# Kernel optimization log

Measured on AMD Instinct MI355X. Metric: run time of the kernel, lower is better.

The kernel has to match this reference:

```python
import jax, jax.numpy as jnp
import numpy as np

B, S, H = 2, 2048, 1024
NQ, NKV, HD, RANK = 16, 4, 64, 8
THETA = 10000.0
LORA_SCALE = 16 / RANK  # alpha / rank = 2.0
ATTN_SCALE = 1.0 / np.sqrt(HD)


def setup_inputs() -> dict:
    key = jax.random.key(0)
    ks = jax.random.split(key, 14)
    n = lambda k, shape, s: jax.random.normal(k, shape, jnp.float32) * s
    return {
        "x": n(ks[0], (B, S, H), 1.0),
        # nn.Linear weights: [out_features, in_features], y = x @ W.T (scaled small for stability)
        "Wq": n(ks[1], (NQ * HD, H), 0.02),
        "Wk": n(ks[2], (NKV * HD, H), 0.02),
        "Wv": n(ks[3], (NKV * HD, H), 0.02),
        "Wo": n(ks[4], (H, NQ * HD), 0.02),
        "qA": n(ks[5], (RANK, H), 0.05), "qB": n(ks[6], (NQ * HD, RANK), 0.05),
        "kA": n(ks[7], (RANK, H), 0.05), "kB": n(ks[8], (NKV * HD, RANK), 0.05),
        "vA": n(ks[9], (RANK, H), 0.05), "vB": n(ks[10], (NKV * HD, RANK), 0.05),
        "oA": n(ks[11], (RANK, NQ * HD), 0.05), "oB": n(ks[12], (H, RANK), 0.05),
    }


def _lora_proj(x, W, A, Bm):
    # x @ W.T + ((x @ A.T) @ B.T) * lora_scaling
    return x @ W.T + ((x @ A.T) @ Bm.T) * LORA_SCALE


def _rope(x, cos_h, sin_h):
    # x: [b, h, s, d]; even/odd interleaved split, concatenated output (matches torch ref)
    x1, x2 = x[..., ::2], x[..., 1::2]
    return jnp.concatenate([x1 * cos_h - x2 * sin_h, x1 * sin_h + x2 * cos_h], axis=-1)


def _forward(x, Wq, Wk, Wv, Wo, qA, qB, kA, kB, vA, vB, oA, oB):
    b, s, _ = x.shape
    q = _lora_proj(x, Wq, qA, qB).reshape(b, s, NQ, HD).transpose(0, 2, 1, 3)
    k = _lora_proj(x, Wk, kA, kB).reshape(b, s, NKV, HD).transpose(0, 2, 1, 3)
    v = _lora_proj(x, Wv, vA, vB).reshape(b, s, NKV, HD).transpose(0, 2, 1, 3)

    inv_freq = 1.0 / (THETA ** (jnp.arange(0, HD, 2, dtype=jnp.float32) / HD))  # [HD/2]
    freqs = jnp.arange(s, dtype=jnp.float32)[:, None] * inv_freq[None, :]  # [s, HD/2]
    cos_h = jnp.cos(freqs)[None, None]  # [1,1,s,HD/2]
    sin_h = jnp.sin(freqs)[None, None]
    q = _rope(q, cos_h, sin_h)
    k = _rope(k, cos_h, sin_h)

    rep = NQ // NKV  # GQA: repeat_interleave along head axis
    k = jnp.repeat(k, rep, axis=1)
    v = jnp.repeat(v, rep, axis=1)

    attn = jax.nn.softmax(jnp.einsum('bhqd,bhkd->bhqk', q, k) * ATTN_SCALE, axis=-1)
    out = jnp.einsum('bhqk,bhkd->bhqd', attn, v)
    out = out.transpose(0, 2, 1, 3).reshape(b, s, NQ * HD)
    return _lora_proj(out, Wo, oA, oB)


def reference(x, Wq, Wk, Wv, Wo, qA, qB, kA, kB, vA, vB, oA, oB):
    return _forward(x, Wq, Wk, Wv, Wo, qA, qB, kA, kB, vA, vB, oA, oB)
```

## Files before the change

kernel.cpp:

```cpp
#include <hip/hip_runtime.h>

typedef _Float16 f16;
typedef __attribute__((ext_vector_type(8))) _Float16 f16x8;
typedef __attribute__((ext_vector_type(4))) float f32x4;

#define DI __device__ __forceinline__
#define MFMA16(a, b, c) __builtin_amdgcn_mfma_f32_16x16x32_f16(a, b, c, 0, 0, 0)

constexpr int BB = 2, SS = 2048, HH = 1024;
constexpr int NQ = 16, NKV = 4, HD = 64;
constexpr int NTOK = BB * SS;
constexpr int NQKV = NQ*HD + 2*NKV*HD;

DI f32x4 zero4() { f32x4 z = {0.f, 0.f, 0.f, 0.f}; return z; }

DI float fexp2(float x) {
#if __has_builtin(__builtin_amdgcn_exp2f)
  return __builtin_amdgcn_exp2f(x);
#else
  return exp2f(x);
#endif
}

DI unsigned pk2(float a, float b) {
#if __has_builtin(__builtin_amdgcn_cvt_pkrtz)
  typedef __fp16 fp16v2 __attribute__((ext_vector_type(2)));
  union { fp16v2 h; unsigned u; } c;
  c.h = __builtin_amdgcn_cvt_pkrtz(a, b);
  return c.u;
#else
  union { f16 h[2]; unsigned u; } c;
  c.h[0] = (f16)a; c.h[1] = (f16)b; return c.u;
#endif
}

DI void glds16(const void* g, void* l) {
  __builtin_amdgcn_global_load_lds((const __attribute__((address_space(1))) void*)g,
                                   (__attribute__((address_space(3))) void*)l, 16, 0, 0);
}

DI int shuf32(int i) {
  return (i & ~31) | (((i >> 2) & 3) << 3) | (i & 3) | (((i >> 4) & 1) << 2);
}

DI void store4h(f16* dst, float4 v) {
  union { f16 h[4]; uint2 u; } o;
  o.h[0] = (f16)v.x; o.h[1] = (f16)v.y; o.h[2] = (f16)v.z; o.h[3] = (f16)v.w;
  *reinterpret_cast<uint2*>(dst) = o.u;
}

__global__ __launch_bounds__(256) void prep_kernel(
    const float* __restrict__ x,
    const float* __restrict__ Wq, const float* __restrict__ Wk,
    const float* __restrict__ Wv, const float* __restrict__ Wo,
    const float* __restrict__ qA, const float* __restrict__ qB,
    const float* __restrict__ kA, const float* __restrict__ kB,
    const float* __restrict__ vA, const float* __restrict__ vB,
    const float* __restrict__ oA, const float* __restrict__ oB,
    f16* __restrict__ xh, f16* __restrict__ Wqkv, f16* __restrict__ Woe,
    float* __restrict__ ctab, float* __restrict__ stab) {
  int u = blockIdx.x * 256 + threadIdx.x;
  if (u < 393216) {
    int e = u << 2;
    int n = e >> 10, hc = e & 1023;
    const float *Am, *Bm; const float* Wsrc; int nn;
    if (n < 1024)      { nn = n;        Wsrc = Wq + e;              Am = qA; Bm = qB; }
    else if (n < 1280) { nn = n - 1024; Wsrc = Wk + nn*1024 + hc;   Am = kA; Bm = kB; }
    else               { nn = n - 1280; Wsrc = Wv + nn*1024 + hc;   Am = vA; Bm = vB; }
    float4 wv = *reinterpret_cast<const float4*>(Wsrc);
    float4 s = {0.f, 0.f, 0.f, 0.f};
#pragma unroll
    for (int r = 0; r < 8; ++r) {
      float bw = 2.0f * Bm[nn*8 + r];
      float4 av = *reinterpret_cast<const float4*>(Am + r*1024 + hc);
      s.x += bw*av.x; s.y += bw*av.y; s.z += bw*av.z; s.w += bw*av.w;
    }
    wv.x += s.x; wv.y += s.y; wv.z += s.z; wv.w += s.w;
    store4h(Wqkv + shuf32(e), wv);
  } else if ((u -= 393216) < 262144) {
    int e = u << 2;
    int n = e >> 10, hc = e & 1023;
    float4 wv = *reinterpret_cast<const float4*>(Wo + e);
    float4 s = {0.f, 0.f, 0.f, 0.f};
#pragma unroll
    for (int r = 0; r < 8; ++r) {
      float bw = 2.0f * oB[n*8 + r];
      float4 av = *reinterpret_cast<const float4*>(oA + r*1024 + hc);
      s.x += bw*av.x; s.y += bw*av.y; s.z += bw*av.z; s.w += bw*av.w;
    }
    wv.x += s.x; wv.y += s.y; wv.z += s.z; wv.w += s.w;
    store4h(Woe + shuf32(e), wv);
  } else if ((u -= 262144) < 1048576) {
    int e = u << 2;
    float4 v = *reinterpret_cast<const float4*>(x + e);
    store4h(xh + shuf32(e), v);
  } else if ((u -= 1048576) < SS * 32) {
    int s = u >> 5, d = u & 31;
    float inv = expf(-(float)d * 0.28782313662425583f);
    float ang = (float)s * inv;
    ctab[u] = cosf(ang);
    stab[u] = sinf(ang);
  }
}

template<typename OUT_T, int BN>
__global__ __launch_bounds__(256, 3) void gemm_bt(const f16* __restrict__ A, const f16* __restrict__ Bw,
                                                  OUT_T* __restrict__ C, int M, int N, int K) {
  constexpr int BUFB = 16384 + BN * 128;
  __shared__ char lds[2 * BUFB];
  const int nt = N / BN;
  const int nwg = (M >> 7) * nt;
  int bid = blockIdx.x;
  const int cpx = nwg >> 3;
  bid = (bid & 7) * cpx + (bid >> 3);
  const int m0 = (bid / nt) << 7;
  const int n0 = (bid % nt) * BN;
  const int tid = threadIdx.x;
  const int lane = tid & 63;
  const int w = tid >> 6;
  const int wr = (BN == 128) ? (w >> 1) : w;
  const int wc = (BN == 128) ? (w & 1) : 0;
  constexpr int MI = (BN == 128) ? 4 : 2;
  const int l15 = lane & 15, g = (lane >> 4) & 3;
  const char* Ab = (const char*)A;
  const char* Bb = (const char*)Bw;
  const size_t Kb = (size_t)K * 2;
  const int srow = tid >> 3;
  const int scol = (tid & 7) << 4;

  auto stage = [&](int kt, int bs) {
    char* ab = lds + bs * BUFB;
    char* bbuf = ab + 16384;
    const size_t kbyte = (size_t)kt << 7;
#pragma unroll
    for (int s = 0; s < 4; ++s) {
      int row = (s << 5) + srow;
      glds16(Ab + (size_t)(m0 + row) * Kb + kbyte + (scol ^ ((row & 7) << 4)),
             ab + (s << 12) + (w << 10));
    }
#pragma unroll
    for (int s = 0; s < BN / 32; ++s) {
      int row = (s << 5) + srow;
      glds16(Bb + (size_t)(n0 + row) * Kb + kbyte + (scol ^ ((row & 7) << 4)),
             bbuf + (s << 12) + (w << 10));
    }
  };

  f32x4 acc[MI][4];
#pragma unroll
  for (int i = 0; i < MI; ++i)
#pragma unroll
    for (int j = 0; j < 4; ++j) acc[i][j] = zero4();

  const int nkt = K >> 6;
  stage(0, 0);
  for (int t = 0; t < nkt; ++t) {
    __syncthreads();
    if (t + 1 < nkt) stage(t + 1, (t + 1) & 1);
    const char* ab = lds + (t & 1) * BUFB;
    const char* bbuf = ab + 16384;
    f16x8 af[MI][2], bf[4][2];
#pragma unroll
    for (int mi = 0; mi < MI; ++mi) {
      int ra = wr * (MI << 4) + (mi << 4) + l15;
      int base = ra << 7, sw = (ra & 7) << 4;
#pragma unroll
      for (int kk = 0; kk < 2; ++kk)
        af[mi][kk] = *reinterpret_cast<const f16x8*>(ab + base + ((((kk << 6) + (g << 4))) ^ sw));
    }
#pragma unroll
    for (int nj = 0; nj < 4; ++nj) {
      int rb = (wc << 6) + (nj << 4) + l15;
      int base = rb << 7, sw = (rb & 7) << 4;
#pragma unroll
      for (int kk = 0; kk < 2; ++kk)
        bf[nj][kk] = *reinterpret_cast<const f16x8*>(bbuf + base + ((((kk << 6) + (g << 4))) ^ sw));
    }
#pragma unroll
    for (int mi = 0; mi < MI; ++mi)
#pragma unroll
      for (int nj = 0; nj < 4; ++nj) {
        acc[mi][nj] = MFMA16(af[mi][0], bf[nj][0], acc[mi][nj]);
        acc[mi][nj] = MFMA16(af[mi][1], bf[nj][1], acc[mi][nj]);
      }
  }
#pragma unroll
  for (int mi = 0; mi < MI; ++mi)
#pragma unroll
    for (int nj = 0; nj < 4; ++nj) {
      int mmb = m0 + wr * (MI << 4) + (mi << 4) + (g << 2);
      int nn  = n0 + (wc << 6) + (nj << 4) + l15;
      f32x4 a = acc[mi][nj];
#pragma unroll
      for (int r = 0; r < 4; ++r) C[(size_t)(mmb + r) * N + nn] = (OUT_T)a[r];
    }
}

__global__ __launch_bounds__(256) void ropev_kernel(const f16* __restrict__ qkv,
    const float* __restrict__ ctab, const float* __restrict__ stab,
    f16* __restrict__ Qr, f16* __restrict__ Kr, f16* __restrict__ Vt) {
  __shared__ f16 Ls[64 * 72];
  if (blockIdx.x < 2560) {
    int u = blockIdx.x * 256 + threadIdx.x;
    int j = u & 7;
    int t = u >> 3;
    int hh = t % 20;
    int tok = t / 20;
    int s = tok & (SS - 1), b = tok >> 11;
    float4 cs = *reinterpret_cast<const float4*>(ctab + (s << 5) + (j << 2));
    float4 sn = *reinterpret_cast<const float4*>(stab + (s << 5) + (j << 2));
    const f16* src = qkv + (size_t)tok * NQKV + (hh < 16 ? hh*64 : 1024 + (hh - 16)*64) + (j << 3);
    union { uint4 q; f16 h[8]; } v;
    v.q = *reinterpret_cast<const uint4*>(src);
    const float sc = hh < 16 ? 0.18033688011112042f : 1.0f;
    f16* out = (hh < 16) ? (Qr + ((size_t)(b*NQ + hh)*SS + s) * HD)
                         : (Kr + ((size_t)(b*NKV + hh - 16)*SS + s) * HD);
    float cc[4] = {cs.x, cs.y, cs.z, cs.w};
    float ss[4] = {sn.x, sn.y, sn.z, sn.w};
    union { f16 h[4]; uint2 u2; } o1, o2;
#pragma unroll
    for (int e = 0; e < 4; ++e) {
      float x1 = (float)v.h[2*e], x2 = (float)v.h[2*e + 1];
      o1.h[e] = (f16)(sc * (x1*cc[e] - x2*ss[e]));
      o2.h[e] = (f16)(sc * (x1*ss[e] + x2*cc[e]));
    }
    int p1b = ((j & 3) << 3) + ((j >> 2) << 2);
    *reinterpret_cast<uint2*>(out + p1b) = o1.u2;
    *reinterpret_cast<uint2*>(out + p1b + 32) = o2.u2;
  } else {
    const int tid = threadIdx.x;
    const int blk = blockIdx.x - 2560;
    const int st = blk & 31, hkv = (blk >> 5) & 3, b = blk >> 7;
    const int s0 = st << 6;
    {
      int s = tid >> 2, d0 = (tid & 3) << 4;
      const f16* src = qkv + ((size_t)(b*SS + s0 + s)) * NQKV + 1280 + hkv*64 + d0;
      uint4 v0 = *reinterpret_cast<const uint4*>(src);
      uint4 v1 = *reinterpret_cast<const uint4*>(src + 8);
      *reinterpret_cast<uint4*>(Ls + s * 72 + d0) = v0;
      *reinterpret_cast<uint4*>(Ls + s * 72 + d0 + 8) = v1;
    }
    __syncthreads();
    int d = tid >> 2;
    f16* dst = Vt + ((size_t)(b*NKV + hkv)*64 + d) * SS + s0;
#pragma unroll
    for (int cc = 0; cc < 2; ++cc) {
      int cch = ((tid & 3) << 1) + cc;
      int m = cch >> 2, g = cch & 3;
      union { f16 h[8]; uint4 u; } o;
#pragma unroll
      for (int j = 0; j < 8; ++j) {
        int sl = (m << 5) + (g << 2) + (j & 3) + ((j >> 2) << 4);
        o.h[j] = Ls[sl * 72 + d];
      }
      *reinterpret_cast<uint4*>(dst + (cch << 3)) = o.u;
    }
  }
}

__global__ __launch_bounds__(512, 4) void attn_kernel(
    const f16* __restrict__ Qr, const f16* __restrict__ Kr,
    const f16* __restrict__ Vt, f16* __restrict__ AO) {
  __shared__ char lds[3 * 16384];
  const int tid = threadIdx.x, lane = tid & 63, w = tid >> 6;
  const int l15 = lane & 15, g = (lane >> 4) & 3;
  const int bh = blockIdx.x;
  const int b = bh >> 4, h = bh & 15, hkv = h >> 2;
  const int q0 = blockIdx.y << 8;
  const char* Kbase = (const char*)(Kr + (size_t)(b*NKV + hkv) * SS * HD);
  const char* Vbase = (const char*)(Vt + (size_t)(b*NKV + hkv) * HD * SS);

  f16x8 qf[2][2];
  {
    const f16* qr0 = Qr + ((size_t)(b*NQ + h)*SS + q0 + (w << 5) + l15) * HD + (g << 3);
    qf[0][0] = *reinterpret_cast<const f16x8*>(qr0);
    qf[0][1] = *reinterpret_cast<const f16x8*>(qr0 + 32);
    qf[1][0] = *reinterpret_cast<const f16x8*>(qr0 + 16*HD);
    qf[1][1] = *reinterpret_cast<const f16x8*>(qr0 + 16*HD + 32);
  }
  f16x8 ones;
#pragma unroll
  for (int i = 0; i < 8; ++i) ones[i] = (f16)1.0f;
  const f32x4 minit = {-4.f, -4.f, -4.f, -4.f};

  f32x4 acc[4][2];
#pragma unroll
  for (int i = 0; i < 4; ++i) { acc[i][0] = zero4(); acc[i][1] = zero4(); }
  f32x4 es0 = zero4(), es1 = zero4();

  f16x8 vreg[4][2];
  union { unsigned u[8]; f16x8 v[2]; } p0, p1;

  const int srow = tid >> 3;
  const int scolb = (tid & 7) << 4;
  auto stage = [&](int kv0, int buf) {
    char* kb = lds + buf * 16384;
    char* vb = kb + 8192;
    glds16(Kbase + (size_t)(kv0 + srow) * 128 + (scolb ^ ((srow & 7) << 4)),
           kb + (w << 10));
    glds16(Vbase + (size_t)srow * 4096 + (kv0 << 1) + (scolb ^ ((srow & 7) << 4)),
           vb + (w << 10));
  };

  stage(0, 0);
  stage(64, 1);
  int cur = 0;

  for (int t = 0; t < 32; ++t) {
    if (t < 31) asm volatile("s_waitcnt vmcnt(2)" ::: "memory");
    else        asm volatile("s_waitcnt vmcnt(0)" ::: "memory");
    __builtin_amdgcn_s_barrier();
    __builtin_amdgcn_sched_barrier(0);
    int nb = cur + 2; if (nb >= 3) nb -= 3;
    if (t + 2 < 32) stage((t + 2) << 6, nb);

    const char* kb = lds + cur * 16384;
    const char* vb = kb + 8192;

    __builtin_amdgcn_s_setprio(1);
    if (t > 0) {
#pragma unroll
      for (int sh = 0; sh < 2; ++sh) {
#pragma unroll
        for (int db = 0; db < 4; ++db) {
          acc[db][0] = MFMA16(vreg[db][sh], p0.v[sh], acc[db][0]);
          acc[db][1] = MFMA16(vreg[db][sh], p1.v[sh], acc[db][1]);
        }
        es0 = MFMA16(ones, p0.v[sh], es0);
        es1 = MFMA16(ones, p1.v[sh], es1);
      }
    }
#pragma unroll
    for (int mb = 0; mb < 4; ++mb) {
      int rowK = (mb << 4) + l15;
      int Bk = (rowK << 7) + ((g << 4) ^ ((rowK & 7) << 4));
      f16x8 kf0 = *reinterpret_cast<const f16x8*>(kb + Bk);
      f16x8 kf1 = *reinterpret_cast<const f16x8*>(kb + (Bk ^ 64));
      f32x4 z0 = minit, z1 = minit;
      z0 = MFMA16(kf0, qf[0][0], z0); z0 = MFMA16(kf1, qf[0][1], z0);
      z1 = MFMA16(kf0, qf[1][0], z1); z1 = MFMA16(kf1, qf[1][1], z1);
      p0.u[(mb << 1)]     = pk2(fexp2(z0[0]), fexp2(z0[1]));
      p0.u[(mb << 1) + 1] = pk2(fexp2(z0[2]), fexp2(z0[3]));
      p1.u[(mb << 1)]     = pk2(fexp2(z1[0]), fexp2(z1[1]));
      p1.u[(mb << 1) + 1] = pk2(fexp2(z1[2]), fexp2(z1[3]));
    }
    __builtin_amdgcn_s_setprio(0);
#pragma unroll
    for (int db = 0; db < 4; ++db) {
      int rowV = (db << 4) + l15;
      int Bv = (rowV << 7) + ((g << 4) ^ ((rowV & 7) << 4));
      vreg[db][0] = *reinterpret_cast<const f16x8*>(vb + Bv);
      vreg[db][1] = *reinterpret_cast<const f16x8*>(vb + (Bv ^ 64));
    }
    cur += 1; if (cur == 3) cur = 0;
  }
#pragma unroll
  for (int sh = 0; sh < 2; ++sh) {
#pragma unroll
    for (int db = 0; db < 4; ++db) {
      acc[db][0] = MFMA16(vreg[db][sh], p0.v[sh], acc[db][0]);
      acc[db][1] = MFMA16(vreg[db][sh], p1.v[sh], acc[db][1]);
    }
    es0 = MFMA16(ones, p0.v[sh], es0);
    es1 = MFMA16(ones, p1.v[sh], es1);
  }

  float i0 = 1.0f / es0[0], i1 = 1.0f / es1[0];
  int sg0 = q0 + (w << 5) + l15;
  size_t ob0 = ((size_t)b * SS + sg0) * 1024 + h * 64;
  size_t ob1 = ob0 + (size_t)16 * 1024;
#pragma unroll
  for (int db = 0; db < 4; ++db) {
    union { f16 hv[4]; uint2 u; } o0, o1;
#pragma unroll
    for (int r = 0; r < 4; ++r) {
      o0.hv[r] = (f16)(acc[db][0][r] * i0);
      o1.hv[r] = (f16)(acc[db][1][r] * i1);
    }
    int pos = ((db >> 1) << 5) + (g << 3) + ((db & 1) << 2);
    *reinterpret_cast<uint2*>(AO + ob0 + pos) = o0.u;
    *reinterpret_cast<uint2*>(AO + ob1 + pos) = o1.u;
  }
}

extern "C" void kernel_launch(void* const* d_in, const int* in_sizes, int n_in,
                              void* d_out, int out_size, void* d_ws, size_t ws_size,
                              hipStream_t stream) {
  const float* x  = (const float*)d_in[0];
  const float* Wq = (const float*)d_in[1];
  const float* Wk = (const float*)d_in[2];
  const float* Wv = (const float*)d_in[3];
  const float* Wo = (const float*)d_in[4];
  const float* qA = (const float*)d_in[5];
  const float* qB = (const float*)d_in[6];
  const float* kA = (const float*)d_in[7];
  const float* kB = (const float*)d_in[8];
  const float* vA = (const float*)d_in[9];
  const float* vB = (const float*)d_in[10];
  const float* oA = (const float*)d_in[11];
  const float* oB = (const float*)d_in[12];
  char* ws = (char*)d_ws;
  f16* xh    = (f16*)(ws);
  f16* Wqkv  = (f16*)(ws + 8388608);
  f16* Woe   = (f16*)(ws + 11534336);
  f16* qkv   = (f16*)(ws + 13631488);
  f16* Qr    = (f16*)(ws + 26214400);
  f16* Kr    = (f16*)(ws + 34603008);
  f16* Vt    = (f16*)(ws + 36700160);
  float* ctab = (float*)(ws + 38797312);
  float* stab = (float*)(ws + 39059456);
  f16* AO = xh;
  float* out = (float*)d_out;

  prep_kernel<<<6912, 256, 0, stream>>>(x, Wq, Wk, Wv, Wo, qA, qB, kA, kB, vA, vB, oA, oB,
                                        xh, Wqkv, Woe, ctab, stab);
  gemm_bt<f16, 64><<<dim3(32 * 24), 256, 0, stream>>>(xh, Wqkv, qkv, 4096, 1536, 1024);
  ropev_kernel<<<2816, 256, 0, stream>>>(qkv, ctab, stab, Qr, Kr, Vt);
  attn_kernel<<<dim3(32, 8), 512, 0, stream>>>(Qr, Kr, Vt, AO);
  gemm_bt<float, 64><<<dim3(32 * 16), 256, 0, stream>>>(AO, Woe, out, 4096, 1024, 1024);
}
```

Measured before the change: 86.26 us.

## Process two KV tiles per iteration with a six-buffer LDS ring

```diff
diff --git a/kernel.cpp b/kernel.cpp
--- a/kernel.cpp
+++ b/kernel.cpp
@@ -258,10 +258,10 @@
   }
 }
 
-__global__ __launch_bounds__(512, 4) void attn_kernel(
+__global__ __launch_bounds__(512, 2) void attn_kernel(
     const f16* __restrict__ Qr, const f16* __restrict__ Kr,
     const f16* __restrict__ Vt, f16* __restrict__ AO) {
-  __shared__ char lds[3 * 16384];
+  __shared__ char lds[6 * 16384];
   const int tid = threadIdx.x, lane = tid & 63, w = tid >> 6;
   const int l15 = lane & 15, g = (lane >> 4) & 3;
   const int bh = blockIdx.x;
@@ -287,9 +287,6 @@
 #pragma unroll
   for (int i = 0; i < 4; ++i) { acc[i][0] = zero4(); acc[i][1] = zero4(); }
   f32x4 es0 = zero4(), es1 = zero4();
-
-  f16x8 vreg[4][2];
-  union { unsigned u[8]; f16x8 v[2]; } p0, p1;
 
   const int srow = tid >> 3;
   const int scolb = (tid & 7) << 4;
@@ -302,67 +299,98 @@
            vb + (w << 10));
   };
 
-  stage(0, 0);
-  stage(64, 1);
-  int cur = 0;
-
-  for (int t = 0; t < 32; ++t) {
-    if (t < 31) asm volatile("s_waitcnt vmcnt(2)" ::: "memory");
+  stage(0, 0); stage(64, 1); stage(128, 2); stage(192, 3);
+
+  int bufA = 0;
+  for (int k = 0; k < 16; ++k) {
+    if (k < 15) asm volatile("s_waitcnt vmcnt(4)" ::: "memory");
     else        asm volatile("s_waitcnt vmcnt(0)" ::: "memory");
     __builtin_amdgcn_s_barrier();
     __builtin_amdgcn_sched_barrier(0);
-    int nb = cur + 2; if (nb >= 3) nb -= 3;
-    if (t + 2 < 32) stage((t + 2) << 6, nb);
-
-    const char* kb = lds + cur * 16384;
-    const char* vb = kb + 8192;
-
+    if (k < 14) {
+      int nb0 = bufA + 4; if (nb0 >= 6) nb0 -= 6;
+      int nb1 = bufA + 5; if (nb1 >= 6) nb1 -= 6;
+      stage((2*k + 4) << 6, nb0);
+      stage((2*k + 5) << 6, nb1);
+    }
+    int bufB = bufA + 1; if (bufB >= 6) bufB -= 6;
+    const char* kbA = lds + bufA * 16384;
+    const char* vbA = kbA + 8192;
+    const char* kbB = lds + bufB * 16384;
+    const char* vbB = kbB + 8192;
+
+    f32x4 sA0[4], sA1[4];
     __builtin_amdgcn_s_setprio(1);
-    if (t > 0) {
-#pragma unroll
-      for (int sh = 0; sh < 2; ++sh) {
-#pragma unroll
-        for (int db = 0; db < 4; ++db) {
-          acc[db][0] = MFMA16(vreg[db][sh], p0.v[sh], acc[db][0]);
-          acc[db][1] = MFMA16(vreg[db][sh], p1.v[sh], acc[db][1]);
-        }
-        es0 = MFMA16(ones, p0.v[sh], es0);
-        es1 = MFMA16(ones, p1.v[sh], es1);
-      }
-    }
 #pragma unroll
     for (int mb = 0; mb < 4; ++mb) {
       int rowK = (mb << 4) + l15;
       int Bk = (rowK << 7) + ((g << 4) ^ ((rowK & 7) << 4));
-      f16x8 kf0 = *reinterpret_cast<const f16x8*>(kb + Bk);
-      f16x8 kf1 = *reinterpret_cast<const f16x8*>(kb + (Bk ^ 64));
+      f16x8 kf0 = *reinterpret_cast<const f16x8*>(kbA + Bk);
+      f16x8 kf1 = *reinterpret_cast<const f16x8*>(kbA + (Bk ^ 64));
       f32x4 z0 = minit, z1 = minit;
       z0 = MFMA16(kf0, qf[0][0], z0); z0 = MFMA16(kf1, qf[0][1], z0);
       z1 = MFMA16(kf0, qf[1][0], z1); z1 = MFMA16(kf1, qf[1][1], z1);
-      p0.u[(mb << 1)]     = pk2(fexp2(z0[0]), fexp2(z0[1]));
-      p0.u[(mb << 1) + 1] = pk2(fexp2(z0[2]), fexp2(z0[3]));
-      p1.u[(mb << 1)]     = pk2(fexp2(z1[0]), fexp2(z1[1]));
-      p1.u[(mb << 1) + 1] = pk2(fexp2(z1[2]), fexp2(z1[3]));
+      sA0[mb] = z0; sA1[mb] = z1;
+    }
+    f32x4 sB0[4], sB1[4];
+#pragma unroll
+    for (int mb = 0; mb < 4; ++mb) {
+      int rowK = (mb << 4) + l15;
+      int Bk = (rowK << 7) + ((g << 4) ^ ((rowK & 7) << 4));
+      f16x8 kf0 = *reinterpret_cast<const f16x8*>(kbB + Bk);
+      f16x8 kf1 = *reinterpret_cast<const f16x8*>(kbB + (Bk ^ 64));
+      f32x4 z0 = minit, z1 = minit;
+      z0 = MFMA16(kf0, qf[0][0], z0); z0 = MFMA16(kf1, qf[0][1], z0);
+      z1 = MFMA16(kf0, qf[1][0], z1); z1 = MFMA16(kf1, qf[1][1], z1);
+      sB0[mb] = z0; sB1[mb] = z1;
     }
     __builtin_amdgcn_s_setprio(0);
-#pragma unroll
-    for (int db = 0; db < 4; ++db) {
-      int rowV = (db << 4) + l15;
-      int Bv = (rowV << 7) + ((g << 4) ^ ((rowV & 7) << 4));
-      vreg[db][0] = *reinterpret_cast<const f16x8*>(vb + Bv);
-      vreg[db][1] = *reinterpret_cast<const f16x8*>(vb + (Bv ^ 64));
-    }
-    cur += 1; if (cur == 3) cur = 0;
-  }
-#pragma unroll
-  for (int sh = 0; sh < 2; ++sh) {
-#pragma unroll
-    for (int db = 0; db < 4; ++db) {
-      acc[db][0] = MFMA16(vreg[db][sh], p0.v[sh], acc[db][0]);
-      acc[db][1] = MFMA16(vreg[db][sh], p1.v[sh], acc[db][1]);
-    }
-    es0 = MFMA16(ones, p0.v[sh], es0);
-    es1 = MFMA16(ones, p1.v[sh], es1);
+    union { unsigned u[8]; f16x8 v[2]; } pA0, pA1;
+#pragma unroll
+    for (int j = 0; j < 8; ++j) {
+      int mb = j >> 1, r0 = (j & 1) << 1;
+      pA0.u[j] = pk2(fexp2(sA0[mb][r0]), fexp2(sA0[mb][r0 + 1]));
+      pA1.u[j] = pk2(fexp2(sA1[mb][r0]), fexp2(sA1[mb][r0 + 1]));
+    }
+    __builtin_amdgcn_s_setprio(1);
+#pragma unroll
+    for (int sh = 0; sh < 2; ++sh) {
+#pragma unroll
+      for (int db = 0; db < 4; ++db) {
+        int rowV = (db << 4) + l15;
+        int Bv = (rowV << 7) + ((g << 4) ^ ((rowV & 7) << 4));
+        f16x8 vf = *reinterpret_cast<const f16x8*>(vbA + (Bv ^ (sh << 6)));
+        acc[db][0] = MFMA16(vf, pA0.v[sh], acc[db][0]);
+        acc[db][1] = MFMA16(vf, pA1.v[sh], acc[db][1]);
+      }
+      es0 = MFMA16(ones, pA0.v[sh], es0);
+      es1 = MFMA16(ones, pA1.v[sh], es1);
+    }
+    __builtin_amdgcn_s_setprio(0);
+    union { unsigned u[8]; f16x8 v[2]; } pB0, pB1;
+#pragma unroll
+    for (int j = 0; j < 8; ++j) {
+      int mb = j >> 1, r0 = (j & 1) << 1;
+      pB0.u[j] = pk2(fexp2(sB0[mb][r0]), fexp2(sB0[mb][r0 + 1]));
+      pB1.u[j] = pk2(fexp2(sB1[mb][r0]), fexp2(sB1[mb][r0 + 1]));
+    }
+    __builtin_amdgcn_s_setprio(1);
+#pragma unroll
+    for (int sh = 0; sh < 2; ++sh) {
+#pragma unroll
+      for (int db = 0; db < 4; ++db) {
+        int rowV = (db << 4) + l15;
+        int Bv = (rowV << 7) + ((g << 4) ^ ((rowV & 7) << 4));
+        f16x8 vf = *reinterpret_cast<const f16x8*>(vbB + (Bv ^ (sh << 6)));
+        acc[db][0] = MFMA16(vf, pB0.v[sh], acc[db][0]);
+        acc[db][1] = MFMA16(vf, pB1.v[sh], acc[db][1]);
+      }
+      es0 = MFMA16(ones, pB0.v[sh], es0);
+      es1 = MFMA16(ones, pB1.v[sh], es1);
+    }
+    __builtin_amdgcn_s_setprio(0);
+
+    bufA += 2; if (bufA >= 6) bufA -= 6;
   }
 
   float i0 = 1.0f / es0[0], i1 = 1.0f / es1[0];
```

Result: no change. 85.67 us, median of 2 (-0.7%).

## Load K/V tiles directly from global into registers, dropping LDS staging

Applied to the files above, without the earlier changes.

```diff
diff --git a/kernel.cpp b/kernel.cpp
--- a/kernel.cpp
+++ b/kernel.cpp
@@ -258,10 +258,9 @@
   }
 }
 
-__global__ __launch_bounds__(512, 4) void attn_kernel(
+__global__ __launch_bounds__(512, 2) void attn_kernel(
     const f16* __restrict__ Qr, const f16* __restrict__ Kr,
     const f16* __restrict__ Vt, f16* __restrict__ AO) {
-  __shared__ char lds[3 * 16384];
   const int tid = threadIdx.x, lane = tid & 63, w = tid >> 6;
   const int l15 = lane & 15, g = (lane >> 4) & 3;
   const int bh = blockIdx.x;
@@ -288,81 +287,67 @@
   for (int i = 0; i < 4; ++i) { acc[i][0] = zero4(); acc[i][1] = zero4(); }
   f32x4 es0 = zero4(), es1 = zero4();
 
-  f16x8 vreg[4][2];
-  union { unsigned u[8]; f16x8 v[2]; } p0, p1;
-
-  const int srow = tid >> 3;
-  const int scolb = (tid & 7) << 4;
-  auto stage = [&](int kv0, int buf) {
-    char* kb = lds + buf * 16384;
-    char* vb = kb + 8192;
-    glds16(Kbase + (size_t)(kv0 + srow) * 128 + (scolb ^ ((srow & 7) << 4)),
-           kb + (w << 10));
-    glds16(Vbase + (size_t)srow * 4096 + (kv0 << 1) + (scolb ^ ((srow & 7) << 4)),
-           vb + (w << 10));
+  auto loadK = [&](int kv0, f16x8 (&kf)[4][2]) {
+#pragma unroll
+    for (int mb = 0; mb < 4; ++mb)
+#pragma unroll
+      for (int kk = 0; kk < 2; ++kk)
+        kf[mb][kk] = *reinterpret_cast<const f16x8*>(
+            Kbase + (size_t)(kv0 + (mb << 4) + l15) * 128 + (kk << 6) + (g << 4));
   };
-
-  stage(0, 0);
-  stage(64, 1);
-  int cur = 0;
-
-  for (int t = 0; t < 32; ++t) {
-    if (t < 31) asm volatile("s_waitcnt vmcnt(2)" ::: "memory");
-    else        asm volatile("s_waitcnt vmcnt(0)" ::: "memory");
-    __builtin_amdgcn_s_barrier();
-    __builtin_amdgcn_sched_barrier(0);
-    int nb = cur + 2; if (nb >= 3) nb -= 3;
-    if (t + 2 < 32) stage((t + 2) << 6, nb);
-
-    const char* kb = lds + cur * 16384;
-    const char* vb = kb + 8192;
-
+  auto loadV = [&](int kv0, f16x8 (&vf)[4][2]) {
+#pragma unroll
+    for (int db = 0; db < 4; ++db)
+#pragma unroll
+      for (int sh = 0; sh < 2; ++sh)
+        vf[db][sh] = *reinterpret_cast<const f16x8*>(
+            Vbase + (size_t)((db << 4) + l15) * 4096 + (kv0 << 1) + (sh << 6) + (g << 4));
+  };
+
+  auto tilestep = [&](const f16x8 (&kf)[4][2], const f16x8 (&vf)[4][2]) {
+    f32x4 sf0[4], sf1[4];
     __builtin_amdgcn_s_setprio(1);
-    if (t > 0) {
-#pragma unroll
-      for (int sh = 0; sh < 2; ++sh) {
-#pragma unroll
-        for (int db = 0; db < 4; ++db) {
-          acc[db][0] = MFMA16(vreg[db][sh], p0.v[sh], acc[db][0]);
-          acc[db][1] = MFMA16(vreg[db][sh], p1.v[sh], acc[db][1]);
-        }
-        es0 = MFMA16(ones, p0.v[sh], es0);
-        es1 = MFMA16(ones, p1.v[sh], es1);
+#pragma unroll
+    for (int mb = 0; mb < 4; ++mb) {
+      f32x4 z0 = minit, z1 = minit;
+      z0 = MFMA16(kf[mb][0], qf[0][0], z0); z0 = MFMA16(kf[mb][1], qf[0][1], z0);
+      z1 = MFMA16(kf[mb][0], qf[1][0], z1); z1 = MFMA16(kf[mb][1], qf[1][1], z1);
+      sf0[mb] = z0; sf1[mb] = z1;
+    }
+    __builtin_amdgcn_s_setprio(0);
+    union { unsigned u[8]; f16x8 v[2]; } p0, p1;
+#pragma unroll
+    for (int j = 0; j < 8; ++j) {
+      int mb = j >> 1, r0 = (j & 1) << 1;
+      p0.u[j] = pk2(fexp2(sf0[mb][r0]), fexp2(sf0[mb][r0 + 1]));
+      p1.u[j] = pk2(fexp2(sf1[mb][r0]), fexp2(sf1[mb][r0 + 1]));
+    }
+    __builtin_amdgcn_s_setprio(1);
+#pragma unroll
+    for (int sh = 0; sh < 2; ++sh) {
+#pragma unroll
+      for (int db = 0; db < 4; ++db) {
+        acc[db][0] = MFMA16(vf[db][sh], p0.v[sh], acc[db][0]);
+        acc[db][1] = MFMA16(vf[db][sh], p1.v[sh], acc[db][1]);
       }
-    }
-#pragma unroll
-    for (int mb = 0; mb < 4; ++mb) {
-      int rowK = (mb << 4) + l15;
-      int Bk = (rowK << 7) + ((g << 4) ^ ((rowK & 7) << 4));
-      f16x8 kf0 = *reinterpret_cast<const f16x8*>(kb + Bk);
-      f16x8 kf1 = *reinterpret_cast<const f16x8*>(kb + (Bk ^ 64));
-      f32x4 z0 = minit, z1 = minit;
-      z0 = MFMA16(kf0, qf[0][0], z0); z0 = MFMA16(kf1, qf[0][1], z0);
-      z1 = MFMA16(kf0, qf[1][0], z1); z1 = MFMA16(kf1, qf[1][1], z1);
-      p0.u[(mb << 1)]     = pk2(fexp2(z0[0]), fexp2(z0[1]));
-      p0.u[(mb << 1) + 1] = pk2(fexp2(z0[2]), fexp2(z0[3]));
-      p1.u[(mb << 1)]     = pk2(fexp2(z1[0]), fexp2(z1[1]));
-      p1.u[(mb << 1) + 1] = pk2(fexp2(z1[2]), fexp2(z1[3]));
+      es0 = MFMA16(ones, p0.v[sh], es0);
+      es1 = MFMA16(ones, p1.v[sh], es1);
     }
     __builtin_amdgcn_s_setprio(0);
-#pragma unroll
-    for (int db = 0; db < 4; ++db) {
-      int rowV = (db << 4) + l15;
-      int Bv = (rowV << 7) + ((g << 4) ^ ((rowV & 7) << 4));
-      vreg[db][0] = *reinterpret_cast<const f16x8*>(vb + Bv);
-      vreg[db][1] = *reinterpret_cast<const f16x8*>(vb + (Bv ^ 64));
-    }
-    cur += 1; if (cur == 3) cur = 0;
-  }
-#pragma unroll
-  for (int sh = 0; sh < 2; ++sh) {
-#pragma unroll
-    for (int db = 0; db < 4; ++db) {
-      acc[db][0] = MFMA16(vreg[db][sh], p0.v[sh], acc[db][0]);
-      acc[db][1] = MFMA16(vreg[db][sh], p1.v[sh], acc[db][1]);
-    }
-    es0 = MFMA16(ones, p0.v[sh], es0);
-    es1 = MFMA16(ones, p1.v[sh], es1);
+  };
+
+  f16x8 kA[4][2], kB[4][2];
+  loadK(0, kA);
+  for (int k = 0; k < 16; ++k) {
+    const int t0 = 2 * k;
+    f16x8 vvA[4][2];
+    loadV(t0 << 6, vvA);
+    loadK((t0 + 1) << 6, kB);
+    tilestep(kA, vvA);
+    f16x8 vvB[4][2];
+    loadV((t0 + 1) << 6, vvB);
+    if (t0 + 2 < 32) loadK((t0 + 2) << 6, kA);
+    tilestep(kB, vvB);
   }
 
   float i0 = 1.0f / es0[0], i1 = 1.0f / es1[0];
```

New measurement: 164.5 us. 90.7% more time.
